# Optimization experiments

Hardware: AMD Instinct MI355X
Metric: run time of the kernel (lower is better)

The kernel has to match this reference:

```python
import jax, jax.numpy as jnp
import numpy as np

D_MODEL = 2048
H_Q = 32
H_KV = 8
D_HEAD = D_MODEL // H_Q   # 64
G = H_Q // H_KV           # 4 query heads per kv head
B, S = 2, 2048


def setup_inputs() -> dict:
    key = jax.random.key(0)
    ks = jax.random.split(key, 7)
    s = 0.02  # weight init scale
    return {
        "q": jax.random.normal(ks[0], (B, S, D_MODEL), jnp.float32),
        "k": jax.random.normal(ks[1], (B, S, D_MODEL), jnp.float32),
        "v": jax.random.normal(ks[2], (B, S, D_MODEL), jnp.float32),
        "Wq": jax.random.normal(ks[3], (D_MODEL, D_MODEL), jnp.float32) * s,
        "Wk": jax.random.normal(ks[4], (D_MODEL, H_KV * D_HEAD), jnp.float32) * s,
        "Wv": jax.random.normal(ks[5], (D_MODEL, H_KV * D_HEAD), jnp.float32) * s,
        "Wo": jax.random.normal(ks[6], (D_MODEL, D_MODEL), jnp.float32) * s,
    }


def reference(q, k, v, Wq, Wk, Wv, Wo):
    # Projections (torch Linear with bias=False: x @ W^T; here W stored as [in,out])
    b, s, _ = q.shape
    # repeat_interleave(k, G, -2) maps kv head j -> query heads j*G..j*G+G-1,
    # i.e. query head h uses kv head h // G. Reshape q heads as (H_KV, G)
    # kv-head-major instead of materializing expanded K/V.
    qh = (q @ Wq).reshape(b, s, H_KV, G, D_HEAD)
    kh = (k @ Wk).reshape(b, s, H_KV, D_HEAD)
    vh = (v @ Wv).reshape(b, s, H_KV, D_HEAD)
    scale = 1.0 / jnp.sqrt(jnp.asarray(D_HEAD, qh.dtype))
    # scores: [B, H_KV, G, Sq, Sk]
    scores = jnp.einsum('bqhgd,bkhd->bhgqk', qh, kh) * scale
    attn = jax.nn.softmax(scores, axis=-1)
    # context: [B, Sq, H_KV, G, D_HEAD]
    ctx = jnp.einsum('bhgqk,bkhd->bqhgd', attn, vh)
    out = ctx.reshape(b, s, D_MODEL) @ Wo
    return out
```

## Files before the change

### kernel.cpp

```cpp
#include <hip/hip_runtime.h>
#include <stdint.h>


typedef __attribute__((ext_vector_type(8))) short short8;
typedef __attribute__((ext_vector_type(4))) float float4v;
typedef __attribute__((ext_vector_type(4))) unsigned short ushort4v;
typedef __attribute__((ext_vector_type(4))) unsigned int uint4v;

__device__ __forceinline__ unsigned short f2bf(float f) {
  union { float f; unsigned int u; } v; v.f = f;
  unsigned int r = v.u + 0x7fffu + ((v.u >> 16) & 1u);
  return (unsigned short)(r >> 16);
}
__device__ __forceinline__ unsigned int fbits(float f) {
  union { float f; unsigned int u; } v; v.f = f; return v.u;
}
__device__ __forceinline__ unsigned int pack_bf16_trunc(float lo, float hi) {
  return __builtin_amdgcn_perm(fbits(hi), fbits(lo), 0x07060302u);
}

__device__ __forceinline__ void gl2lds16(const unsigned short* g, unsigned short* l) {
  __builtin_amdgcn_global_load_lds(
      (const __attribute__((address_space(1))) void*)g,
      (__attribute__((address_space(3))) void*)l, 16, 0, 0);
}

__global__ void prep(const float* __restrict__ q, const float* __restrict__ k,
                     const float* __restrict__ v,
                     const float* __restrict__ Wq, const float* __restrict__ Wk,
                     const float* __restrict__ Wv,
                     unsigned short* __restrict__ qb, unsigned short* __restrict__ kb,
                     unsigned short* __restrict__ vb,
                     unsigned short* __restrict__ WTq, unsigned short* __restrict__ WTk,
                     unsigned short* __restrict__ WTv)
{
  __shared__ unsigned short t[32][33];
  const int z = blockIdx.z;
  if (z >= 3) {
    const float* in  = (z == 3) ? q : (z == 4) ? k : v;
    unsigned short* out = (z == 3) ? qb : (z == 4) ? kb : vb;
    const int tid = threadIdx.y * 32 + threadIdx.x;
    const int bid = blockIdx.y * 64 + blockIdx.x;
    for (int i = bid * 256 + tid; i < 2097152; i += 4096 * 256) {
      const float4v a = *(const float4v*)(in + (size_t)i * 4);
      *(ushort4v*)(out + (size_t)i * 4) = (ushort4v){f2bf(a.x), f2bf(a.y), f2bf(a.z), f2bf(a.w)};
    }
    return;
  }
  const float* in; unsigned short* out; int R, C;
  if (z == 0)      { in = Wq; out = WTq; R = 2048; C = 2048; }
  else if (z == 1) { in = Wk; out = WTk; R = 2048; C = 512; }
  else             { in = Wv; out = WTv; R = 2048; C = 512; }
  const int x0 = blockIdx.x * 32, y0 = blockIdx.y * 32;
  if (x0 >= C) return;
  const int tx = threadIdx.x, ty = threadIdx.y;
#pragma unroll
  for (int i = 0; i < 4; ++i) {
    const int r = y0 + ty + i * 8, c = x0 + tx;
    t[ty + i * 8][tx] = f2bf(in[(size_t)r * C + c]);
  }
  __syncthreads();
#pragma unroll
  for (int i = 0; i < 4; ++i)
    out[(size_t)(x0 + ty + i * 8) * R + y0 + tx] = t[tx][ty + i * 8];
}

template<int TN, bool C_BF16>
__device__ void gemm_body(const unsigned short* __restrict__ A,
                          const unsigned short* __restrict__ Bt,
                          void* __restrict__ C, int N, int K, float cscale,
                          int bx, int by)
{
  constexpr int NT = TN / 32;
  __shared__ unsigned short As[128][64];
  __shared__ unsigned short Bs[TN][64];

  const int tid  = threadIdx.x;
  const int wave = tid >> 6;
  const int lane = tid & 63;
  const int quad = lane >> 4;
  const int l15  = lane & 15;
  const int wm   = (wave >> 1) * 64;
  const int wn   = (wave & 1) * (TN / 2);
  const int m0   = by * 128;
  const int n0   = bx * TN;

  const int r8  = lane >> 3;
  const int lc8 = ((lane & 7) ^ r8) * 8;

  float4v acc[4][NT];
#pragma unroll
  for (int i = 0; i < 4; ++i)
#pragma unroll
    for (int j = 0; j < NT; ++j) acc[i][j] = (float4v)0.0f;

  for (int k0 = 0; k0 < K; k0 += 64) {
    __syncthreads();
#pragma unroll
    for (int i = 0; i < 4; ++i) {
      const int rb = i * 32 + wave * 8;
      gl2lds16(A + (size_t)(m0 + rb + r8) * K + k0 + lc8, &As[rb][0]);
    }
#pragma unroll
    for (int i = 0; i < TN / 32; ++i) {
      const int rb = i * 32 + wave * 8;
      gl2lds16(Bt + (size_t)(n0 + rb + r8) * K + k0 + lc8, &Bs[rb][0]);
    }
    __syncthreads();

#pragma unroll
    for (int kk = 0; kk < 2; ++kk) {
      const int cx = kk * 4 + quad;
      short8 af[4], bf[NT];
#pragma unroll
      for (int mt = 0; mt < 4; ++mt)
        af[mt] = *(const short8*)&As[wm + mt * 16 + l15][(cx ^ (l15 & 7)) * 8];
#pragma unroll
      for (int nt = 0; nt < NT; ++nt)
        bf[nt] = *(const short8*)&Bs[wn + nt * 16 + l15][(cx ^ (l15 & 7)) * 8];
#pragma unroll
      for (int mt = 0; mt < 4; ++mt)
#pragma unroll
        for (int nt = 0; nt < NT; ++nt)
          acc[mt][nt] = __builtin_amdgcn_mfma_f32_16x16x32_bf16(af[mt], bf[nt], acc[mt][nt], 0, 0, 0);
    }
  }

#pragma unroll
  for (int mt = 0; mt < 4; ++mt)
#pragma unroll
    for (int nt = 0; nt < NT; ++nt) {
      const int row = m0 + wm + mt * 16 + quad * 4;
      const int col = n0 + wn + nt * 16 + l15;
#pragma unroll
      for (int r = 0; r < 4; ++r) {
        const float val = acc[mt][nt][r] * cscale;
        if (C_BF16) ((unsigned short*)C)[(size_t)(row + r) * N + col] = f2bf(val);
        else        ((float*)C)[(size_t)(row + r) * N + col] = val;
      }
    }
}

__global__ __launch_bounds__(256, 2)
void gemm_mid(const unsigned short* __restrict__ qb, const unsigned short* __restrict__ WTq,
              unsigned short* __restrict__ Qp,
              const unsigned short* __restrict__ kb, const unsigned short* __restrict__ WTk,
              unsigned short* __restrict__ Kp,
              const unsigned short* __restrict__ WTv, const unsigned short* __restrict__ vb,
              unsigned short* __restrict__ VpT, float sm_scale)
{
  const int id = blockIdx.x;
  if (id < 512) {
    const int s = (id & 7) * 64 + (id >> 3);
    gemm_body<128, true>(qb, WTq, Qp, 2048, 2048, sm_scale, s & 15, s >> 4);
  } else if (id < 768) {
    const int t = id - 512;
    const int s = (t & 7) * 32 + (t >> 3);
    gemm_body<64, true>(kb, WTk, Kp, 512, 2048, 1.0f, s & 7, s >> 3);
  } else {
    const int t = id - 768;
    const int s = (t & 7) * 32 + (t >> 3);
    gemm_body<64, true>(WTv, vb, VpT, 4096, 2048, 1.0f, s & 63, s >> 6);
  }
}

template<int TN, bool C_BF16, int GX>
__global__ __launch_bounds__(256, 2)
void gemm_swz(const unsigned short* __restrict__ A, const unsigned short* __restrict__ Bt,
              void* __restrict__ C, int N, int K, float cscale)
{
  const int chunk = gridDim.x >> 3;
  const int s = (blockIdx.x & 7) * chunk + (blockIdx.x >> 3);
  gemm_body<TN, C_BF16>(A, Bt, C, N, K, cscale, s % GX, s / GX);
}

__global__ __launch_bounds__(256, 4)
void attn_flash(const unsigned short* __restrict__ Qp,
                const unsigned short* __restrict__ Kp,
                const unsigned short* __restrict__ VpT,
                unsigned short* __restrict__ Ctx,
                const float* __restrict__ Wo,
                unsigned short* __restrict__ WTo)
{
  __shared__ unsigned short Ks[2][64 * 64];
  __shared__ unsigned short VTs[2][64 * 64];

  const int tid  = threadIdx.x;
  const int wave = tid >> 6;
  const int lane = tid & 63;
  const int quad = lane >> 4;
  const int l15  = lane & 15;

  const int head = blockIdx.y;
  const int b    = head >> 5;
  const int hq   = head & 31;
  const int hkv  = hq >> 2;
  const size_t qrow = (size_t)(b * 2048 + blockIdx.x * 128 + wave * 32);

  short8 qf[2][2];
#pragma unroll
  for (int mt = 0; mt < 2; ++mt)
#pragma unroll
    for (int kc = 0; kc < 2; ++kc)
      qf[mt][kc] = *(const short8*)&Qp[(qrow + mt * 16 + l15) * 2048 + hq * 64 + kc * 32 + quad * 8];

  float4v oa[2][4];
  float4v lacc[2];
#pragma unroll
  for (int mt = 0; mt < 2; ++mt) {
    lacc[mt] = (float4v)0.0f;
#pragma unroll
    for (int dt = 0; dt < 4; ++dt) oa[mt][dt] = (float4v)0.0f;
  }
  short8 ones;
#pragma unroll
  for (int i = 0; i < 8; ++i) ones[i] = (short)0x3F80;

  auto stage = [&](int j, int bu) {
#pragma unroll
    for (int i = 0; i < 2; ++i) {
      const int s  = i * 256 + wave * 64 + lane;
      const int r  = s >> 3;
      const int lc = (s & 7) ^ (r & 7);
      const int rk = ((r >> 4) & 1) * 32 + ((r >> 2) & 3) * 8 + (r >> 5) * 4 + (r & 3);
      gl2lds16(Kp + (size_t)(b * 2048 + j * 64 + rk) * 512 + hkv * 64 + lc * 8,
               &Ks[bu][i * 2048 + wave * 512]);
      gl2lds16(VpT + (size_t)(hkv * 64 + r) * 4096 + b * 2048 + j * 64 + lc * 8,
               &VTs[bu][i * 2048 + wave * 512]);
    }
  };

  stage(0, 0);
  __syncthreads();

  for (int j = 0; j < 32; ++j) {
    const int bu = j & 1;
    if (j < 31) stage(j + 1, bu ^ 1);

    short8 kf[4][2];
#pragma unroll
    for (int nt = 0; nt < 4; ++nt) {
      const int krow = nt * 16 + l15;
      kf[nt][0] = *(const short8*)&Ks[bu][krow * 64 + ((quad ^ (l15 & 7)) * 8)];
      kf[nt][1] = *(const short8*)&Ks[bu][krow * 64 + (((4 + quad) ^ (l15 & 7)) * 8)];
    }

    __builtin_amdgcn_s_setprio(1);

    unsigned int w[2][4][2];
#pragma unroll
    for (int mt = 0; mt < 2; ++mt) {
#pragma unroll
      for (int nt = 0; nt < 4; ++nt) {
        float4v sa = (float4v)0.0f;
        sa = __builtin_amdgcn_mfma_f32_16x16x32_bf16(kf[nt][0], qf[mt][0], sa, 0, 0, 0);
        sa = __builtin_amdgcn_mfma_f32_16x16x32_bf16(kf[nt][1], qf[mt][1], sa, 0, 0, 0);
        const float e0 = __builtin_amdgcn_exp2f(sa[0]);
        const float e1 = __builtin_amdgcn_exp2f(sa[1]);
        const float e2 = __builtin_amdgcn_exp2f(sa[2]);
        const float e3 = __builtin_amdgcn_exp2f(sa[3]);
        w[mt][nt][0] = pack_bf16_trunc(e0, e1);
        w[mt][nt][1] = pack_bf16_trunc(e2, e3);
      }
    }

#pragma unroll
    for (int kc = 0; kc < 2; ++kc) {
      union { uint4v u; short8 s; } p0u, p1u;
      p0u.u = (uint4v){w[0][kc][0], w[0][kc][1], w[0][kc + 2][0], w[0][kc + 2][1]};
      p1u.u = (uint4v){w[1][kc][0], w[1][kc][1], w[1][kc + 2][0], w[1][kc + 2][1]};
      const short8 pf0 = p0u.s;
      const short8 pf1 = p1u.s;
#pragma unroll
      for (int dt = 0; dt < 4; ++dt) {
        const int vrow = dt * 16 + l15;
        const short8 vf = *(const short8*)&VTs[bu][vrow * 64 + (((kc * 4 + quad) ^ (l15 & 7)) * 8)];
        oa[0][dt] = __builtin_amdgcn_mfma_f32_16x16x32_bf16(pf0, vf, oa[0][dt], 0, 0, 0);
        oa[1][dt] = __builtin_amdgcn_mfma_f32_16x16x32_bf16(pf1, vf, oa[1][dt], 0, 0, 0);
      }
      lacc[0] = __builtin_amdgcn_mfma_f32_16x16x32_bf16(pf0, ones, lacc[0], 0, 0, 0);
      lacc[1] = __builtin_amdgcn_mfma_f32_16x16x32_bf16(pf1, ones, lacc[1], 0, 0, 0);
    }

    __builtin_amdgcn_s_setprio(0);
    __syncthreads();
  }

#pragma unroll
  for (int mt = 0; mt < 2; ++mt)
#pragma unroll
    for (int r = 0; r < 4; ++r) {
      const float inv = 1.0f / lacc[mt][r];
#pragma unroll
      for (int dt = 0; dt < 4; ++dt)
        Ctx[(qrow + mt * 16 + quad * 4 + r) * 2048 + hq * 64 + dt * 16 + l15] =
            f2bf(oa[mt][dt][r] * inv);
    }

  {
    unsigned short (*t)[33] = (unsigned short (*)[33])&Ks[0][0];
    const int bid = blockIdx.y * 16 + blockIdx.x;
    const int tx = tid & 31, ty = tid >> 5;
#pragma unroll
    for (int tt = 0; tt < 4; ++tt) {
      const int tile = bid * 4 + tt;
      const int x0 = (tile & 63) * 32, y0 = (tile >> 6) * 32;
#pragma unroll
      for (int i = 0; i < 4; ++i)
        t[ty + i * 8][tx] = f2bf(Wo[(size_t)(y0 + ty + i * 8) * 2048 + x0 + tx]);
      __syncthreads();
#pragma unroll
      for (int i = 0; i < 4; ++i)
        WTo[(size_t)(x0 + ty + i * 8) * 2048 + y0 + tx] = t[tx][ty + i * 8];
      __syncthreads();
    }
  }
}

extern "C" void kernel_launch(void* const* d_in, const int* in_sizes, int n_in,
                              void* d_out, int out_size, void* d_ws, size_t ws_size,
                              hipStream_t stream)
{
  const float* q  = (const float*)d_in[0];
  const float* k  = (const float*)d_in[1];
  const float* v  = (const float*)d_in[2];
  const float* Wq = (const float*)d_in[3];
  const float* Wk = (const float*)d_in[4];
  const float* Wv = (const float*)d_in[5];
  const float* Wo = (const float*)d_in[6];
  float* out = (float*)d_out;

  unsigned short* ws  = (unsigned short*)d_ws;
  unsigned short* qb  = ws;
  unsigned short* kb  = qb  + (size_t)8388608;
  unsigned short* vb  = kb  + (size_t)8388608;
  unsigned short* WT  = vb  + (size_t)8388608;
  unsigned short* Qp  = WT  + (size_t)4194304;
  unsigned short* Kp  = Qp  + (size_t)8388608;
  unsigned short* VpT = Kp  + (size_t)2097152;
  unsigned short* Ctx = qb;
  unsigned short* WTk = (unsigned short*)d_out;
  unsigned short* WTv = (unsigned short*)d_out + 1048576;

  const dim3 blk(256);
  const dim3 tblk(32, 8);
  const float SM_SCALE = 0.125f * 1.44269504089f;

  prep<<<dim3(64, 64, 6), tblk, 0, stream>>>(q, k, v, Wq, Wk, Wv,
                                             qb, kb, vb, WT, WTk, WTv);

  gemm_mid<<<dim3(1024), blk, 0, stream>>>(qb, WT, Qp, kb, WTk, Kp, WTv, vb, VpT, SM_SCALE);

  attn_flash<<<dim3(16, 64), blk, 0, stream>>>(Qp, Kp, VpT, Ctx, Wo, WT);

  gemm_swz<128, false, 16><<<dim3(512), blk, 0, stream>>>(Ctx, WT, out, 2048, 2048, 1.0f);
}
```

Baseline: 342.5 us.

## Double-buffer GEMM LDS tiles and move Wo transpose into prep kernel

The shared GEMM body now uses two LDS buffers for A and B, loading the next k-tile while the current one feeds the MFMAs, with a single barrier per step. This aims to hide global load latency behind matrix math. When the workspace is large enough, the Wo transpose-to-bf16 runs in the prep kernel instead of the attention kernel's tail. The cost is doubled LDS use per GEMM block, which may reduce occupancy, and reliance on the barrier to order the async LDS loads.

```diff
diff --git a/kernel.cpp b/kernel.cpp
--- a/kernel.cpp
+++ b/kernel.cpp
@@ -28,15 +28,15 @@
 __global__ void prep(const float* __restrict__ q, const float* __restrict__ k,
                      const float* __restrict__ v,
                      const float* __restrict__ Wq, const float* __restrict__ Wk,
-                     const float* __restrict__ Wv,
+                     const float* __restrict__ Wv, const float* __restrict__ Wo,
                      unsigned short* __restrict__ qb, unsigned short* __restrict__ kb,
                      unsigned short* __restrict__ vb,
                      unsigned short* __restrict__ WTq, unsigned short* __restrict__ WTk,
-                     unsigned short* __restrict__ WTv)
+                     unsigned short* __restrict__ WTv, unsigned short* __restrict__ WTo)
 {
   __shared__ unsigned short t[32][33];
   const int z = blockIdx.z;
-  if (z >= 3) {
+  if (z >= 3 && z <= 5) {
     const float* in  = (z == 3) ? q : (z == 4) ? k : v;
     unsigned short* out = (z == 3) ? qb : (z == 4) ? kb : vb;
     const int tid = threadIdx.y * 32 + threadIdx.x;
@@ -50,7 +50,8 @@
   const float* in; unsigned short* out; int R, C;
   if (z == 0)      { in = Wq; out = WTq; R = 2048; C = 2048; }
   else if (z == 1) { in = Wk; out = WTk; R = 2048; C = 512; }
-  else             { in = Wv; out = WTv; R = 2048; C = 512; }
+  else if (z == 2) { in = Wv; out = WTv; R = 2048; C = 512; }
+  else             { in = Wo; out = WTo; R = 2048; C = 2048; }
   const int x0 = blockIdx.x * 32, y0 = blockIdx.y * 32;
   if (x0 >= C) return;
   const int tx = threadIdx.x, ty = threadIdx.y;
@@ -72,8 +73,8 @@
                           int bx, int by)
 {
   constexpr int NT = TN / 32;
-  __shared__ unsigned short As[128][64];
-  __shared__ unsigned short Bs[TN][64];
+  __shared__ unsigned short As[2][128][64];
+  __shared__ unsigned short Bs[2][TN][64];
 
   const int tid  = threadIdx.x;
   const int wave = tid >> 6;
@@ -88,25 +89,32 @@
   const int r8  = lane >> 3;
   const int lc8 = ((lane & 7) ^ r8) * 8;
 
-  float4v acc[4][NT];
-#pragma unroll
-  for (int i = 0; i < 4; ++i)
-#pragma unroll
-    for (int j = 0; j < NT; ++j) acc[i][j] = (float4v)0.0f;
-
-  for (int k0 = 0; k0 < K; k0 += 64) {
-    __syncthreads();
+  auto stage = [&](int k0, int bu) {
 #pragma unroll
     for (int i = 0; i < 4; ++i) {
       const int rb = i * 32 + wave * 8;
-      gl2lds16(A + (size_t)(m0 + rb + r8) * K + k0 + lc8, &As[rb][0]);
+      gl2lds16(A + (size_t)(m0 + rb + r8) * K + k0 + lc8, &As[bu][rb][0]);
     }
 #pragma unroll
     for (int i = 0; i < TN / 32; ++i) {
       const int rb = i * 32 + wave * 8;
-      gl2lds16(Bt + (size_t)(n0 + rb + r8) * K + k0 + lc8, &Bs[rb][0]);
-    }
-    __syncthreads();
+      gl2lds16(Bt + (size_t)(n0 + rb + r8) * K + k0 + lc8, &Bs[bu][rb][0]);
+    }
+  };
+
+  float4v acc[4][NT];
+#pragma unroll
+  for (int i = 0; i < 4; ++i)
+#pragma unroll
+    for (int j = 0; j < NT; ++j) acc[i][j] = (float4v)0.0f;
+
+  stage(0, 0);
+  __syncthreads();
+
+  const int nsteps = K >> 6;
+  for (int t = 0; t < nsteps; ++t) {
+    const int bu = t & 1;
+    if (t + 1 < nsteps) stage((t + 1) << 6, bu ^ 1);
 
 #pragma unroll
     for (int kk = 0; kk < 2; ++kk) {
@@ -114,16 +122,17 @@
       short8 af[4], bf[NT];
 #pragma unroll
       for (int mt = 0; mt < 4; ++mt)
-        af[mt] = *(const short8*)&As[wm + mt * 16 + l15][(cx ^ (l15 & 7)) * 8];
+        af[mt] = *(const short8*)&As[bu][wm + mt * 16 + l15][(cx ^ (l15 & 7)) * 8];
 #pragma unroll
       for (int nt = 0; nt < NT; ++nt)
-        bf[nt] = *(const short8*)&Bs[wn + nt * 16 + l15][(cx ^ (l15 & 7)) * 8];
+        bf[nt] = *(const short8*)&Bs[bu][wn + nt * 16 + l15][(cx ^ (l15 & 7)) * 8];
 #pragma unroll
       for (int mt = 0; mt < 4; ++mt)
 #pragma unroll
         for (int nt = 0; nt < NT; ++nt)
           acc[mt][nt] = __builtin_amdgcn_mfma_f32_16x16x32_bf16(af[mt], bf[nt], acc[mt][nt], 0, 0, 0);
     }
+    __syncthreads();
   }
 
 #pragma unroll
@@ -180,7 +189,8 @@
                 const unsigned short* __restrict__ VpT,
                 unsigned short* __restrict__ Ctx,
                 const float* __restrict__ Wo,
-                unsigned short* __restrict__ WTo)
+                unsigned short* __restrict__ WTo,
+                int doTail)
 {
   __shared__ unsigned short Ks[2][64 * 64];
   __shared__ unsigned short VTs[2][64 * 64];
@@ -297,7 +307,7 @@
             f2bf(oa[mt][dt][r] * inv);
     }
 
-  {
+  if (doTail) {
     unsigned short (*t)[33] = (unsigned short (*)[33])&Ks[0][0];
     const int bid = blockIdx.y * 16 + blockIdx.x;
     const int tx = tid & 31, ty = tid >> 5;
@@ -338,20 +348,25 @@
   unsigned short* Qp  = WT  + (size_t)4194304;
   unsigned short* Kp  = Qp  + (size_t)8388608;
   unsigned short* VpT = Kp  + (size_t)2097152;
+  unsigned short* WTo_ws = VpT + (size_t)2097152;
   unsigned short* Ctx = qb;
   unsigned short* WTk = (unsigned short*)d_out;
   unsigned short* WTv = (unsigned short*)d_out + 1048576;
 
+  const bool woInPrep = ws_size >= (size_t)(41943040 + 4194304) * 2;
+  unsigned short* WTo = woInPrep ? WTo_ws : WT;
+
   const dim3 blk(256);
   const dim3 tblk(32, 8);
   const float SM_SCALE = 0.125f * 1.44269504089f;
 
-  prep<<<dim3(64, 64, 6), tblk, 0, stream>>>(q, k, v, Wq, Wk, Wv,
-                                             qb, kb, vb, WT, WTk, WTv);
+  prep<<<dim3(64, 64, woInPrep ? 7 : 6), tblk, 0, stream>>>(
+      q, k, v, Wq, Wk, Wv, Wo, qb, kb, vb, WT, WTk, WTv, WTo_ws);
 
   gemm_mid<<<dim3(1024), blk, 0, stream>>>(qb, WT, Qp, kb, WTk, Kp, WTv, vb, VpT, SM_SCALE);
 
-  attn_flash<<<dim3(16, 64), blk, 0, stream>>>(Qp, Kp, VpT, Ctx, Wo, WT);
-
-  gemm_swz<128, false, 16><<<dim3(512), blk, 0, stream>>>(Ctx, WT, out, 2048, 2048, 1.0f);
-}
+  attn_flash<<<dim3(16, 64), blk, 0, stream>>>(Qp, Kp, VpT, Ctx, Wo, WT,
+                                               woInPrep ? 0 : 1);
+
+  gemm_swz<128, false, 16><<<dim3(512), blk, 0, stream>>>(Ctx, WTo, out, 2048, 2048, 1.0f);
+}
```

After: 410.7 us. 19.9% more time.
